# Kernel tuning notes

Hardware: AMD Instinct MI355X
Metric: run time of the kernel (lower is better)

Reference implementation:

```python
import jax, jax.numpy as jnp
import numpy as np

N = 64      # SSM state size (hidden_size)
H = 1024    # channels
L = 2048    # sequence length
BATCH = 8


def setup_inputs() -> dict:
    key = jax.random.key(0)
    ks = jax.random.split(key, 12)
    s = 1.0 / np.sqrt(N)
    n = jnp.arange(N, dtype=jnp.float32)
    return {
        "r": jax.random.normal(ks[0], (BATCH, L, H), dtype=jnp.float32),
        "B_re": jax.random.normal(ks[1], (N,), dtype=jnp.float32) * s,
        "B_im": jax.random.normal(ks[2], (N,), dtype=jnp.float32) * s,
        "C_re": jax.random.normal(ks[3], (H, N), dtype=jnp.float32) * s,
        "C_im": jax.random.normal(ks[4], (H, N), dtype=jnp.float32) * s,
        "P_re": jax.random.normal(ks[5], (N,), dtype=jnp.float32) * s,
        "P_im": jax.random.normal(ks[6], (N,), dtype=jnp.float32) * s,
        "Q_re": jax.random.normal(ks[7], (N,), dtype=jnp.float32) * s,
        "Q_im": jax.random.normal(ks[8], (N,), dtype=jnp.float32) * s,
        # HiPPO-LegS-like diagonal: negative real part for stability, imag ~ pi*n
        "diag_re": -0.5 * jnp.ones((N,), dtype=jnp.float32),
        "diag_im": jnp.pi * (n - N / 2.0),
        "step": jnp.array([1e-3], dtype=jnp.float32),
        "D": jnp.zeros((1,), dtype=jnp.float32),
    }


def _dplr_kernel(Bc, Cc, Pc, Qc, Lam, step, seq_len):
    # Standard S4 DPLR generating function evaluated at roots of unity,
    # then inverse FFT -> real convolution kernel K_c of shape (H, L).
    z = jnp.exp(-2j * jnp.pi * jnp.arange(seq_len) / seq_len).astype(jnp.complex64)  # (L,)
    g = (2.0 / step) * (1.0 - z) / (1.0 + z)                                          # (L,)
    cden = 1.0 / (g[:, None] - Lam[None, :])                                          # (L,N) Cauchy denom
    k00 = jnp.einsum('hn,ln->hl', Cc * Bc, cden)   # (H,L)
    k01 = jnp.einsum('hn,ln->hl', Cc * Pc, cden)   # (H,L)
    k10 = jnp.einsum('n,ln->l', Qc * Bc, cden)     # (L,)
    k11 = jnp.einsum('n,ln->l', Qc * Pc, cden)     # (L,)
    at_roots = (2.0 / (1.0 + z)) * (k00 - k01 * (k10 / (1.0 + k11)))  # (H,L)
    return jnp.fft.ifft(at_roots, axis=-1).real


def reference(r, B_re, B_im, C_re, C_im, P_re, P_im, Q_re, Q_im,
              diag_re, diag_im, step, D):
    step_c = jnp.maximum(step[0], 1e-6)
    Bc = B_re + 1j * B_im
    Cc = C_re + 1j * C_im
    Pc = P_re + 1j * P_im
    Qc = Q_re + 1j * Q_im
    Lam = diag_re + 1j * diag_im
    seq_len = r.shape[1]
    K = _dplr_kernel(Bc, Cc, Pc, Qc, Lam, step_c, seq_len)  # (H, L)
    # causal FFT convolution along the sequence axis
    nfft = 2 * seq_len
    Kf = jnp.fft.rfft(K, n=nfft, axis=-1)            # (H, nfft//2+1)
    uf = jnp.fft.rfft(r, n=nfft, axis=1)             # (B, nfft//2+1, H)
    h1 = jnp.fft.irfft(uf * Kf.T[None], n=nfft, axis=1)[:, :seq_len]  # (B,L,H)
    y1 = h1 + D[0] * r
    return jax.nn.gelu(y1, approximate=False)
```

## Files before the change

kernel.cpp:

```cpp
#include <hip/hip_runtime.h>
#include <math.h>

#define SSM_N 64
#define SSM_H 1024
#define SSM_L 2048
#define SSM_B 8
#define FFTN 2048
#define NT 256
#define NT2 512

#define PSWZ(a) ((a) ^ (((a) >> 4) & 15))

typedef float f2 __attribute__((ext_vector_type(2)));
static __device__ __forceinline__ f2 mkf2(float a, float b){ f2 v; v.x = a; v.y = b; return v; }

static __device__ __forceinline__ f2 cmul(f2 a, f2 b){
  return mkf2(-a.y, a.y) * mkf2(b.y, b.x) + mkf2(a.x, a.x) * b;
}
static __device__ __forceinline__ f2 cconj(f2 a){ return mkf2(a.x, -a.y); }

template<bool INV> static __device__ __forceinline__ f2 mul_mi(f2 a){
  return INV ? mkf2(-a.y, a.x) : mkf2(a.y, -a.x);
}
template<bool INV> static __device__ __forceinline__ f2 mul_w81(f2 a){
  const float r = 0.70710678118654752440f;
  return INV ? (r * mkf2(a.x - a.y, a.y + a.x)) : (r * mkf2(a.x + a.y, a.y - a.x));
}
template<bool INV> static __device__ __forceinline__ f2 mul_w83(f2 a){
  const float r = 0.70710678118654752440f;
  return INV ? (r * mkf2(-(a.x + a.y), a.x - a.y)) : (r * mkf2(a.y - a.x, -(a.x + a.y)));
}

#define W8C0 1.f
#define W8S0 0.f
#define W8C1 0.92387953251f
#define W8S1 (-0.38268343236f)
#define W8C2 0.70710678119f
#define W8S2 (-0.70710678119f)
#define W8C3 0.38268343236f
#define W8S3 (-0.92387953251f)
#define W8C4 0.f
#define W8S4 (-1.f)
#define W8C5 (-0.38268343236f)
#define W8S5 (-0.92387953251f)
#define W8C6 (-0.70710678119f)
#define W8S6 (-0.70710678119f)
#define W8C7 (-0.92387953251f)
#define W8S7 (-0.38268343236f)

template<bool INV>
static __device__ __forceinline__ void bfly8(const f2* x, f2* y)
{
  f2 t0=x[0]+x[4], t4=x[0]-x[4];
  f2 t1=x[1]+x[5], t5=x[1]-x[5];
  f2 t2=x[2]+x[6], t6=x[2]-x[6];
  f2 t3=x[3]+x[7], t7=x[3]-x[7];
  f2 b0=t0+t2, b2=t0-t2, b1=t1+t3, b3=t1-t3;
  f2 mb3 = mul_mi<INV>(b3);
  y[0]=b0+b1; y[4]=b0-b1; y[2]=b2+mb3; y[6]=b2-mb3;
  f2 v1 = mul_w81<INV>(t5), v2 = mul_mi<INV>(t6), v3 = mul_w83<INV>(t7);
  f2 a0=t4+v2, a2=t4-v2, a1=v1+v3, a3=v1-v3;
  f2 ma3 = mul_mi<INV>(a3);
  y[1]=a0+a1; y[5]=a0-a1; y[3]=a2+ma3; y[7]=a2-ma3;
}

template<bool INV>
static __device__ __forceinline__ void calc_w8(const f2* __restrict__ tw, int j, f2* w)
{
  f2 w1 = tw[j];
  if (INV) w1.y = -w1.y;
  w[1]=w1; w[2]=cmul(w1,w1); w[3]=cmul(w[2],w1); w[4]=cmul(w[2],w[2]);
  w[5]=cmul(w[3],w[2]); w[6]=cmul(w[3],w[3]); w[7]=cmul(w[4],w[3]);
}

static __device__ __forceinline__ void twstore(f2* __restrict__ dst, const f2* y, const f2* w,
                                               int base, int S)
{
  dst[PSWZ(base)]     = y[0];
  dst[PSWZ(base+S)]   = cmul(y[1],w[1]);
  dst[PSWZ(base+2*S)] = cmul(y[2],w[2]);
  dst[PSWZ(base+3*S)] = cmul(y[3],w[3]);
  dst[PSWZ(base+4*S)] = cmul(y[4],w[4]);
  dst[PSWZ(base+5*S)] = cmul(y[5],w[5]);
  dst[PSWZ(base+6*S)] = cmul(y[6],w[6]);
  dst[PSWZ(base+7*S)] = cmul(y[7],w[7]);
}

template<bool INV>
static __device__ __forceinline__ void bfly8_store(f2* __restrict__ dst, const f2* __restrict__ tw,
                                                   f2* x, int j, int base, int S)
{
  f2 y[8]; bfly8<INV>(x, y);
  f2 w[8]; calc_w8<INV>(tw, j, w);
  twstore(dst, y, w, base, S);
}

template<bool INV, bool ZTOP>
static __device__ __forceinline__ void stage8_first(const f2* __restrict__ src, f2* __restrict__ dst,
                                                    const f2* __restrict__ tw, int t, int st)
{
  const f2* sp = src + st;
  f2 x[8];
  if (ZTOP) {
    #pragma unroll
    for (int q = 0; q < 4; ++q) { x[q] = sp[256*q]; x[q+4] = mkf2(0.f, 0.f); }
  } else {
    #pragma unroll
    for (int q = 0; q < 8; ++q) x[q] = sp[256*q];
  }
  bfly8_store<INV>(dst, tw, x, t, t*8, 1);
}

template<bool INV, int S>
static __device__ __forceinline__ void stage8_mid(const f2* __restrict__ src, f2* __restrict__ dst,
                                                  const f2* __restrict__ tw, int t, int st)
{
  const f2* sp = src + st;
  f2 x[8];
  #pragma unroll
  for (int q = 0; q < 8; ++q) x[q] = sp[256*q];
  int i = t & (S-1);
  int j = t - i;
  bfly8_store<INV>(dst, tw, x, j, i + j*8, S);
}

template<bool INV, int S>
static __device__ __forceinline__ void stage8_mid_ip(f2* __restrict__ buf, const f2* __restrict__ tw,
                                                     int t, int st)
{
  f2 x[8];
  #pragma unroll
  for (int q = 0; q < 8; ++q) x[q] = buf[st + 256*q];
  __syncthreads();
  int i = t & (S-1);
  int j = t - i;
  bfly8_store<INV>(buf, tw, x, j, i + j*8, S);
  __syncthreads();
}

template<bool INV, bool HALFOUT>
static __device__ __forceinline__ void stage4f(const f2* __restrict__ src, f2* __restrict__ dst, int st)
{
  #pragma unroll
  for (int hh = 0; hh < 2; ++hh) {
    const f2* sp = src + st + 256*hh;
    f2* wp = dst + st + 256*hh;
    f2 x0=sp[0], x1=sp[512], x2=sp[1024], x3=sp[1536];
    f2 a0=x0+x2, a2=x0-x2, a1=x1+x3, a3=x1-x3;
    f2 m = mul_mi<INV>(a3);
    wp[0]   = a0+a1;
    wp[512] = a2+m;
    if (!HALFOUT) {
      wp[1024] = a0-a1;
      wp[1536] = a2-m;
    }
  }
}

template<bool INV>
static __device__ __forceinline__ void stage4f_ip(f2* __restrict__ buf, int st)
{
  f2 xr[2][4];
  #pragma unroll
  for (int hh = 0; hh < 2; ++hh) {
    const f2* sp = buf + st + 256*hh;
    xr[hh][0]=sp[0]; xr[hh][1]=sp[512]; xr[hh][2]=sp[1024]; xr[hh][3]=sp[1536];
  }
  __syncthreads();
  #pragma unroll
  for (int hh = 0; hh < 2; ++hh) {
    f2* wp = buf + st + 256*hh;
    f2 a0=xr[hh][0]+xr[hh][2], a2=xr[hh][0]-xr[hh][2];
    f2 a1=xr[hh][1]+xr[hh][3], a3=xr[hh][1]-xr[hh][3];
    f2 m = mul_mi<INV>(a3);
    wp[0]    = a0+a1;
    wp[512]  = a2+m;
    wp[1024] = a0-a1;
    wp[1536] = a2-m;
  }
  __syncthreads();
}

template<bool INV>
static __device__ __forceinline__ void stage4f_reg(const f2* __restrict__ src, f2* out, int st)
{
  #pragma unroll
  for (int hh = 0; hh < 2; ++hh) {
    const f2* sp = src + st + 256*hh;
    f2 x0=sp[0], x1=sp[512], x2=sp[1024], x3=sp[1536];
    f2 a0=x0+x2, a2=x0-x2, a1=x1+x3, a3=x1-x3;
    f2 m = mul_mi<INV>(a3);
    out[hh]   = a0+a1;
    out[hh+2] = a2+m;
    out[hh+4] = a0-a1;
    out[hh+6] = a2-m;
  }
}

static __device__ __forceinline__ f2 init_tw(f2* tw, int t)
{
  float s, c;
  sincosf(-6.2831853071795864769f * (float)t / (float)FFTN, &s, &c);
  f2 v = mkf2(c, s);
  tw[t] = v;
  return v;
}

__global__ __launch_bounds__(256) void kprep(
    const float* __restrict__ r, float* __restrict__ rT,
    const float* __restrict__ B_re, const float* __restrict__ B_im,
    const float* __restrict__ P_re, const float* __restrict__ P_im,
    const float* __restrict__ Q_re, const float* __restrict__ Q_im,
    const float* __restrict__ diag_re, const float* __restrict__ diag_im,
    const float* __restrict__ step,
    f2* __restrict__ cdenT, f2* __restrict__ f2v, f2* __restrict__ facv)
{
  __shared__ float til[64][65];
  int bid = blockIdx.x;
  int t = threadIdx.x;
  if (bid < 4096) {
    int tx = t & 15, ty = t >> 4;
    int h0 = (bid & 15) * 64, l0 = ((bid >> 4) & 31) * 64, b = bid >> 9;
    const float4* s4 = (const float4*)(r + ((size_t)b*SSM_L + l0)*SSM_H + h0);
    #pragma unroll
    for (int i = 0; i < 4; ++i) {
      int lr = ty + 16*i;
      float4 v = s4[(size_t)lr*(SSM_H/4) + tx];
      til[lr][4*tx+0]=v.x; til[lr][4*tx+1]=v.y; til[lr][4*tx+2]=v.z; til[lr][4*tx+3]=v.w;
    }
    __syncthreads();
    float4* d4 = (float4*)(rT + ((size_t)b*SSM_H + h0)*SSM_L + l0);
    #pragma unroll
    for (int i = 0; i < 4; ++i) {
      int hr = ty + 16*i;
      float4 w;
      w.x = til[4*tx+0][hr]; w.y = til[4*tx+1][hr];
      w.z = til[4*tx+2][hr]; w.w = til[4*tx+3][hr];
      d4[(size_t)hr*(SSM_L/4) + tx] = w;
    }
  } else {
    int gid = (bid - 4096) * 256 + t;
    int l = gid >> 3, s = gid & 7;
    double stepc = (double)step[0]; if (stepc < 1e-6) stepc = 1e-6;
    double ang = -2.0 * 3.14159265358979323846 * (double)l / (double)SSM_L;
    double zr = cos(ang), zi = sin(ang);
    double dr = 1.0 + zr, di = zi;
    double nr = 1.0 - zr, ni = -zi;
    double den = dr*dr + di*di;
    double i2s = 2.0 / stepc;
    double gr = i2s * (nr*dr + ni*di) / den;
    double gi = i2s * (ni*dr - nr*di) / den;
    double k10r=0.0, k10i=0.0, k11r=0.0, k11i=0.0;
    #pragma unroll
    for (int q = 0; q < 8; ++q) {
      int n = s*8 + q;
      double ar = gr - (double)diag_re[n];
      double ai = gi - (double)diag_im[n];
      double d2 = ar*ar + ai*ai;
      double cr = ar/d2, ci = -ai/d2;
      cdenT[n*SSM_L + l] = mkf2((float)cr, (float)ci);
      double qr = (double)Q_re[n], qi = (double)Q_im[n];
      double br = (double)B_re[n], bi = (double)B_im[n];
      double pr = (double)P_re[n], pi = (double)P_im[n];
      double qbr = qr*br - qi*bi, qbi = qr*bi + qi*br;
      double qpr = qr*pr - qi*pi, qpi = qr*pi + qi*pr;
      k10r += qbr*cr - qbi*ci; k10i += qbr*ci + qbi*cr;
      k11r += qpr*cr - qpi*ci; k11i += qpr*ci + qpi*cr;
    }
    #pragma unroll
    for (int off = 1; off < 8; off <<= 1) {
      k10r += __shfl_xor(k10r, off);
      k10i += __shfl_xor(k10i, off);
      k11r += __shfl_xor(k11r, off);
      k11i += __shfl_xor(k11i, off);
    }
    if (s == 0) {
      f2v[l] = mkf2((float)(2.0*dr/den), (float)(-2.0*di/den));
      double er = 1.0 + k11r, ei = k11i;
      double ed = er*er + ei*ei;
      facv[l] = mkf2((float)((k10r*er + k10i*ei)/ed), (float)((k10i*er - k10r*ei)/ed));
    }
  }
}

__global__ __launch_bounds__(NT2, 4) void kkern(
    const float* __restrict__ C_re, const float* __restrict__ C_im,
    const float* __restrict__ B_re, const float* __restrict__ B_im,
    const float* __restrict__ P_re, const float* __restrict__ P_im,
    const f2* __restrict__ cdenT, const f2* __restrict__ f2v, const f2* __restrict__ facv,
    float4* __restrict__ PQg)
{
  __shared__ f2 bufA[2][FFTN];
  __shared__ f2 bufB[2][FFTN];
  __shared__ f2 tw[256];
  int t = threadIdx.x;
  int tt = t & 255, ch = t >> 8, stt = PSWZ(tt);
  int h0 = blockIdx.x * 2;
  if (t < 256) init_tw(tw, t);
  f2* cbs = bufA[0];
  if (t < 128) {
    int h = h0 + (t >> 6), n = t & 63;
    f2 cc = mkf2(C_re[h*SSM_N + n], C_im[h*SSM_N + n]);
    cbs[t]       = cmul(cc, mkf2(B_re[n], B_im[n]));
    cbs[128 + t] = cmul(cc, mkf2(P_re[n], P_im[n]));
  }
  __syncthreads();
  f2 k00[2][4], k01[2][4];
  #pragma unroll
  for (int h2 = 0; h2 < 2; ++h2)
    #pragma unroll
    for (int i = 0; i < 4; ++i) { k00[h2][i] = mkf2(0.f,0.f); k01[h2][i] = mkf2(0.f,0.f); }
  f2 cd[4];
  #pragma unroll
  for (int i = 0; i < 4; ++i) cd[i] = cdenT[t + i*NT2];
  for (int n = 0; n < SSM_N; ++n) {
    f2 cdn[4];
    #pragma unroll
    for (int i = 0; i < 4; ++i) cdn[i] = cdenT[((n+1)&63)*SSM_L + t + i*NT2];
    #pragma unroll
    for (int h2 = 0; h2 < 2; ++h2) {
      f2 cb = cbs[h2*64 + n], cp = cbs[128 + h2*64 + n];
      #pragma unroll
      for (int i = 0; i < 4; ++i) {
        k00[h2][i] = k00[h2][i] + cmul(cb, cd[i]);
        k01[h2][i] = k01[h2][i] + cmul(cp, cd[i]);
      }
    }
    #pragma unroll
    for (int i = 0; i < 4; ++i) cd[i] = cdn[i];
  }
  __syncthreads();
  #pragma unroll
  for (int h2 = 0; h2 < 2; ++h2)
    #pragma unroll
    for (int i = 0; i < 4; ++i) {
      int l = t + i*NT2;
      f2 fv = f2v[l], fc = facv[l];
      bufA[h2][PSWZ(l)] = cmul(fv, k00[h2][i] - cmul(k01[h2][i], fc));
    }
  __syncthreads();
  f2* A  = bufA[ch];
  f2* Bb = bufB[ch];
  f2 ebin[4], e2048 = mkf2(0.f, 0.f);
  #pragma unroll
  for (int i = 0; i < 4; ++i) {
    int m = tt + i*256;
    if (m == 0) {
      ebin[0] = mkf2(A[0].x, 0.f);
      e2048   = mkf2(A[PSWZ(FFTN/2)].x, 0.f);
    } else {
      ebin[i] = 0.5f * (A[PSWZ(m)] + cconj(A[PSWZ(FFTN - m)]));
    }
  }
  stage8_first<true, false>(A, Bb, tw, tt, stt);
  __syncthreads();
  stage8_mid<true, 8>(Bb, A, tw, tt, stt);
  __syncthreads();
  stage8_mid<true, 64>(A, Bb, tw, tt, stt);
  __syncthreads();
  {
    f2 kr[8];
    stage4f_reg<true>(Bb, kr, stt);
    float sbb, cbb;
    sincosf(-3.14159265358979f * (float)tt / (float)FFTN, &sbb, &cbb);
    f2 cbase = mkf2(cbb, sbb);
    const float Wc8[8] = {W8C0,W8C1,W8C2,W8C3,W8C4,W8C5,W8C6,W8C7};
    const float Ws8[8] = {W8S0,W8S1,W8S2,W8S3,W8S4,W8S5,W8S6,W8S7};
    const float scale = 1.0f / (float)FFTN;
    #pragma unroll
    for (int q = 0; q < 8; ++q) {
      f2 tq = cmul(cbase, mkf2(Wc8[q], Ws8[q]));
      kr[q] = (kr[q].x * scale) * tq;
    }
    f2 w[8]; calc_w8<false>(tw, tt, w);
    f2 y[8]; bfly8<false>(kr, y); twstore(A, y, w, tt*8, 1);
  }
  __syncthreads();
  stage8_mid<false, 8>(A, Bb, tw, tt, stt);
  __syncthreads();
  stage8_mid<false, 64>(Bb, A, tw, tt, stt);
  __syncthreads();
  stage4f<false, true>(A, Bb, stt);
  #pragma unroll
  for (int i = 0; i < 4; ++i) {
    int m = tt + 256*i;
    f2 v = ebin[i];
    if (m == 0) v = e2048;
    Bb[1024 + m] = v;
  }
  __syncthreads();
  f2 u = tw[tt];
  const float q4 = 1.0f / 4096.0f;
  const f2 c1 = mkf2(0.99999882345170176f, -0.00153398018628477f);
  f2 base_odd = cmul(c1, u);
  const float Wc8[8] = {W8C0,W8C1,W8C2,W8C3,W8C4,W8C5,W8C6,W8C7};
  const float Ws8[8] = {W8S0,W8S1,W8S2,W8S3,W8S4,W8S5,W8S6,W8S7};
  float4* pqrow = PQg + (size_t)(h0 + ch) * FFTN;
  #pragma unroll
  for (int i = 0; i < 4; ++i) {
    int m = tt + 256*i;
    f2 Ka = ebin[i];
    f2 Kb = Bb[1024 + ((1024 - m) & 1023)];
    f2 ee = cmul(u, mkf2(Wc8[2*i], Ws8[2*i]));
    float cv = ee.x, sv = -ee.y;
    float am = q4*(1.f - sv), ap = q4*(1.f + sv), cq = q4*cv;
    f2 P = mkf2(Ka.x*am + Kb.x*ap, Ka.y*am - Kb.y*ap);
    f2 dd = mkf2(Ka.x - Kb.x, Ka.y + Kb.y);
    pqrow[2*m] = make_float4(P.x, P.y, -dd.y*cq, dd.x*cq);
    f2 Ko = Bb[PSWZ(m)];
    f2 Kp = Bb[PSWZ(1023 - m)];
    f2 eo = cmul(base_odd, mkf2(Wc8[2*i], Ws8[2*i]));
    cv = eo.x; sv = -eo.y;
    am = q4*(1.f - sv); ap = q4*(1.f + sv); cq = q4*cv;
    f2 P2 = mkf2(Ko.x*am + Kp.x*ap, Ko.y*am - Kp.y*ap);
    f2 d2 = mkf2(Ko.x - Kp.x, Ko.y + Kp.y);
    pqrow[2*m+1] = make_float4(P2.x, P2.y, -d2.y*cq, d2.x*cq);
  }
}

__global__ __launch_bounds__(NT, 4) void kconv(float* __restrict__ rT,
                                               const float4* __restrict__ PQg,
                                               const float* __restrict__ Dp)
{
  __shared__ f2 buf[FFTN];
  __shared__ f2 tw[256];
  int t = threadIdx.x, st = PSWZ(t);
  int xc = blockIdx.x & 7, y = blockIdx.x >> 3;
  int h = xc * 128 + (y >> 3);
  int b = y & 7;
  float Dv = Dp[0];
  init_tw(tw, t);
  float* rrow = rT + ((size_t)b*SSM_H + h) * SSM_L;
  const f2* r2 = (const f2*)rrow;
  f2 rv[4];
  #pragma unroll
  for (int i = 0; i < 4; ++i) rv[i] = r2[t + i*NT];
  {
    f2 xx[8];
    #pragma unroll
    for (int q = 0; q < 4; ++q) { xx[q] = rv[q]; xx[q+4] = mkf2(0.f, 0.f); }
    bfly8_store<false>(buf, tw, xx, t, t*8, 1);
  }
  __syncthreads();
  stage8_mid_ip<false, 8>(buf, tw, t, st);
  stage8_mid_ip<false, 64>(buf, tw, t, st);
  const float4* pqrow = PQg + (size_t)h * FFTN;
  float4 pq[8];
  #pragma unroll
  for (int i = 0; i < 8; ++i) pq[i] = pqrow[t + i*NT];
  stage4f_ip<false>(buf, st);
  {
    f2 xx[8];
    #pragma unroll
    for (int i = 0; i < 8; ++i) {
      int k = t + i*NT;
      int kk = (FFTN - k) & (FFTN - 1);
      f2 Ck  = buf[st + i*NT];
      f2 Ckk = buf[PSWZ(kk)];
      xx[i] = cmul(mkf2(pq[i].x, pq[i].y), Ck) + cmul(mkf2(pq[i].z, pq[i].w), cconj(Ckk));
    }
    __syncthreads();
    bfly8_store<true>(buf, tw, xx, t, t*8, 1);
  }
  __syncthreads();
  stage8_mid_ip<true, 8>(buf, tw, t, st);
  stage8_mid_ip<true, 64>(buf, tw, t, st);
  f2* o2 = (f2*)rrow;
  #pragma unroll
  for (int hh = 0; hh < 2; ++hh) {
    const f2* sp = buf + st + 256*hh;
    f2 x0=sp[0], x1=sp[512], x2=sp[1024], x3=sp[1536];
    f2 a0=x0+x2, a2=x0-x2, a1=x1+x3, a3=x1-x3;
    f2 mm = mul_mi<true>(a3);
    f2 y0 = a0+a1, y1 = a2+mm;
    f2 rA = rv[hh], rB = rv[hh+2];
    o2[t + 256*hh]       = mkf2(y0.x + Dv*rA.x, y0.y + Dv*rA.y);
    o2[t + 256*hh + 512] = mkf2(y1.x + Dv*rB.x, y1.y + Dv*rB.y);
  }
}

__global__ __launch_bounds__(256) void ktback(const float* __restrict__ yT, float* __restrict__ out)
{
  __shared__ float til[64][65];
  int t = threadIdx.x, tx = t & 15, ty = t >> 4;
  int h0 = blockIdx.x * 64, l0 = blockIdx.y * 64, b = blockIdx.z;
  const float4* s4 = (const float4*)(yT + ((size_t)b*SSM_H + h0)*SSM_L + l0);
  #pragma unroll
  for (int i = 0; i < 4; ++i) {
    int hr = ty + 16*i;
    float4 v = s4[(size_t)hr*(SSM_L/4) + tx];
    til[hr][4*tx+0]=v.x; til[hr][4*tx+1]=v.y; til[hr][4*tx+2]=v.z; til[hr][4*tx+3]=v.w;
  }
  __syncthreads();
  float4* d4 = (float4*)(out + ((size_t)b*SSM_L + l0)*SSM_H + h0);
  #pragma unroll
  for (int i = 0; i < 4; ++i) {
    int lr = ty + 16*i;
    float4 w;
    float x0 = til[4*tx+0][lr], x1 = til[4*tx+1][lr];
    float x2 = til[4*tx+2][lr], x3 = til[4*tx+3][lr];
    w.x = 0.5f * x0 * (1.0f + erff(x0 * 0.70710678118654752f));
    w.y = 0.5f * x1 * (1.0f + erff(x1 * 0.70710678118654752f));
    w.z = 0.5f * x2 * (1.0f + erff(x2 * 0.70710678118654752f));
    w.w = 0.5f * x3 * (1.0f + erff(x3 * 0.70710678118654752f));
    d4[(size_t)lr*(SSM_H/4) + tx] = w;
  }
}

extern "C" void kernel_launch(void* const* d_in, const int* in_sizes, int n_in,
                              void* d_out, int out_size, void* d_ws, size_t ws_size,
                              hipStream_t stream)
{
  const float* r       = (const float*)d_in[0];
  const float* B_re    = (const float*)d_in[1];
  const float* B_im    = (const float*)d_in[2];
  const float* C_re    = (const float*)d_in[3];
  const float* C_im    = (const float*)d_in[4];
  const float* P_re    = (const float*)d_in[5];
  const float* P_im    = (const float*)d_in[6];
  const float* Q_re    = (const float*)d_in[7];
  const float* Q_im    = (const float*)d_in[8];
  const float* diag_re = (const float*)d_in[9];
  const float* diag_im = (const float*)d_in[10];
  const float* step    = (const float*)d_in[11];
  const float* Dp      = (const float*)d_in[12];
  float* out = (float*)d_out;

  char* p = (char*)d_ws;
  float* rT  = (float*)p;  p += (size_t)SSM_B*SSM_H*SSM_L*sizeof(float);
  f2* cdenT  = (f2*)p;     p += (size_t)SSM_N*SSM_L*sizeof(f2);
  f2* f2v    = (f2*)p;     p += (size_t)SSM_L*sizeof(f2);
  f2* facv   = (f2*)p;     p += (size_t)SSM_L*sizeof(f2);
  float4* PQ = (float4*)p; p += (size_t)SSM_H*FFTN*sizeof(float4);

  kprep<<<4096 + 64, 256, 0, stream>>>(r, rT, B_re, B_im, P_re, P_im, Q_re, Q_im,
                                       diag_re, diag_im, step, cdenT, f2v, facv);
  kkern<<<SSM_H/2, NT2, 0, stream>>>(C_re, C_im, B_re, B_im, P_re, P_im,
                                     cdenT, f2v, facv, PQ);
  kconv<<<SSM_B*SSM_H, NT, 0, stream>>>(rT, PQ, Dp);
  ktback<<<dim3(SSM_H/64, SSM_L/64, SSM_B), 256, 0, stream>>>(rT, out);
}
```

Measured before the change: 264.7 us.

## Drop transpose kernels; read and write strided rows directly in conv kernel

```diff
diff --git a/kernel.cpp b/kernel.cpp
--- a/kernel.cpp
+++ b/kernel.cpp
@@ -207,7 +207,6 @@
 }
 
 __global__ __launch_bounds__(256) void kprep(
-    const float* __restrict__ r, float* __restrict__ rT,
     const float* __restrict__ B_re, const float* __restrict__ B_im,
     const float* __restrict__ P_re, const float* __restrict__ P_im,
     const float* __restrict__ Q_re, const float* __restrict__ Q_im,
@@ -215,71 +214,46 @@
     const float* __restrict__ step,
     f2* __restrict__ cdenT, f2* __restrict__ f2v, f2* __restrict__ facv)
 {
-  __shared__ float til[64][65];
-  int bid = blockIdx.x;
-  int t = threadIdx.x;
-  if (bid < 4096) {
-    int tx = t & 15, ty = t >> 4;
-    int h0 = (bid & 15) * 64, l0 = ((bid >> 4) & 31) * 64, b = bid >> 9;
-    const float4* s4 = (const float4*)(r + ((size_t)b*SSM_L + l0)*SSM_H + h0);
-    #pragma unroll
-    for (int i = 0; i < 4; ++i) {
-      int lr = ty + 16*i;
-      float4 v = s4[(size_t)lr*(SSM_H/4) + tx];
-      til[lr][4*tx+0]=v.x; til[lr][4*tx+1]=v.y; til[lr][4*tx+2]=v.z; til[lr][4*tx+3]=v.w;
-    }
-    __syncthreads();
-    float4* d4 = (float4*)(rT + ((size_t)b*SSM_H + h0)*SSM_L + l0);
-    #pragma unroll
-    for (int i = 0; i < 4; ++i) {
-      int hr = ty + 16*i;
-      float4 w;
-      w.x = til[4*tx+0][hr]; w.y = til[4*tx+1][hr];
-      w.z = til[4*tx+2][hr]; w.w = til[4*tx+3][hr];
-      d4[(size_t)hr*(SSM_L/4) + tx] = w;
-    }
-  } else {
-    int gid = (bid - 4096) * 256 + t;
-    int l = gid >> 3, s = gid & 7;
-    double stepc = (double)step[0]; if (stepc < 1e-6) stepc = 1e-6;
-    double ang = -2.0 * 3.14159265358979323846 * (double)l / (double)SSM_L;
-    double zr = cos(ang), zi = sin(ang);
-    double dr = 1.0 + zr, di = zi;
-    double nr = 1.0 - zr, ni = -zi;
-    double den = dr*dr + di*di;
-    double i2s = 2.0 / stepc;
-    double gr = i2s * (nr*dr + ni*di) / den;
-    double gi = i2s * (ni*dr - nr*di) / den;
-    double k10r=0.0, k10i=0.0, k11r=0.0, k11i=0.0;
-    #pragma unroll
-    for (int q = 0; q < 8; ++q) {
-      int n = s*8 + q;
-      double ar = gr - (double)diag_re[n];
-      double ai = gi - (double)diag_im[n];
-      double d2 = ar*ar + ai*ai;
-      double cr = ar/d2, ci = -ai/d2;
-      cdenT[n*SSM_L + l] = mkf2((float)cr, (float)ci);
-      double qr = (double)Q_re[n], qi = (double)Q_im[n];
-      double br = (double)B_re[n], bi = (double)B_im[n];
-      double pr = (double)P_re[n], pi = (double)P_im[n];
-      double qbr = qr*br - qi*bi, qbi = qr*bi + qi*br;
-      double qpr = qr*pr - qi*pi, qpi = qr*pi + qi*pr;
-      k10r += qbr*cr - qbi*ci; k10i += qbr*ci + qbi*cr;
-      k11r += qpr*cr - qpi*ci; k11i += qpr*ci + qpi*cr;
-    }
-    #pragma unroll
-    for (int off = 1; off < 8; off <<= 1) {
-      k10r += __shfl_xor(k10r, off);
-      k10i += __shfl_xor(k10i, off);
-      k11r += __shfl_xor(k11r, off);
-      k11i += __shfl_xor(k11i, off);
-    }
-    if (s == 0) {
-      f2v[l] = mkf2((float)(2.0*dr/den), (float)(-2.0*di/den));
-      double er = 1.0 + k11r, ei = k11i;
-      double ed = er*er + ei*ei;
-      facv[l] = mkf2((float)((k10r*er + k10i*ei)/ed), (float)((k10i*er - k10r*ei)/ed));
-    }
+  int gid = blockIdx.x * 256 + threadIdx.x;
+  int l = gid >> 3, s = gid & 7;
+  double stepc = (double)step[0]; if (stepc < 1e-6) stepc = 1e-6;
+  double ang = -2.0 * 3.14159265358979323846 * (double)l / (double)SSM_L;
+  double zr = cos(ang), zi = sin(ang);
+  double dr = 1.0 + zr, di = zi;
+  double nr = 1.0 - zr, ni = -zi;
+  double den = dr*dr + di*di;
+  double i2s = 2.0 / stepc;
+  double gr = i2s * (nr*dr + ni*di) / den;
+  double gi = i2s * (ni*dr - nr*di) / den;
+  double k10r=0.0, k10i=0.0, k11r=0.0, k11i=0.0;
+  #pragma unroll
+  for (int q = 0; q < 8; ++q) {
+    int n = s*8 + q;
+    double ar = gr - (double)diag_re[n];
+    double ai = gi - (double)diag_im[n];
+    double d2 = ar*ar + ai*ai;
+    double cr = ar/d2, ci = -ai/d2;
+    cdenT[n*SSM_L + l] = mkf2((float)cr, (float)ci);
+    double qr = (double)Q_re[n], qi = (double)Q_im[n];
+    double br = (double)B_re[n], bi = (double)B_im[n];
+    double pr = (double)P_re[n], pi = (double)P_im[n];
+    double qbr = qr*br - qi*bi, qbi = qr*bi + qi*br;
+    double qpr = qr*pr - qi*pi, qpi = qr*pi + qi*pr;
+    k10r += qbr*cr - qbi*ci; k10i += qbr*ci + qbi*cr;
+    k11r += qpr*cr - qpi*ci; k11i += qpr*ci + qpi*cr;
+  }
+  #pragma unroll
+  for (int off = 1; off < 8; off <<= 1) {
+    k10r += __shfl_xor(k10r, off);
+    k10i += __shfl_xor(k10i, off);
+    k11r += __shfl_xor(k11r, off);
+    k11i += __shfl_xor(k11i, off);
+  }
+  if (s == 0) {
+    f2v[l] = mkf2((float)(2.0*dr/den), (float)(-2.0*di/den));
+    double er = 1.0 + k11r, ei = k11i;
+    double ed = er*er + ei*ei;
+    facv[l] = mkf2((float)((k10r*er + k10i*ei)/ed), (float)((k10i*er - k10r*ei)/ed));
   }
 }
 
@@ -418,23 +392,26 @@
   }
 }
 
-__global__ __launch_bounds__(NT, 4) void kconv(float* __restrict__ rT,
+__global__ __launch_bounds__(NT, 4) void kconv(const float* __restrict__ r,
                                                const float4* __restrict__ PQg,
-                                               const float* __restrict__ Dp)
+                                               const float* __restrict__ Dp,
+                                               float* __restrict__ out)
 {
   __shared__ f2 buf[FFTN];
   __shared__ f2 tw[256];
   int t = threadIdx.x, st = PSWZ(t);
-  int xc = blockIdx.x & 7, y = blockIdx.x >> 3;
-  int h = xc * 128 + (y >> 3);
-  int b = y & 7;
+  int xcd = blockIdx.x & 7, local = blockIdx.x >> 3;
+  int h = (xcd << 7) | (local & 127);
+  int b = local >> 7;
   float Dv = Dp[0];
+  const float* rp = r + (size_t)b * SSM_L * SSM_H + h;
+  f2 rv[4];
+  #pragma unroll
+  for (int i = 0; i < 4; ++i) {
+    int j2 = t + i*NT;
+    rv[i] = mkf2(rp[(size_t)(2*j2) * SSM_H], rp[(size_t)(2*j2 + 1) * SSM_H]);
+  }
   init_tw(tw, t);
-  float* rrow = rT + ((size_t)b*SSM_H + h) * SSM_L;
-  const f2* r2 = (const f2*)rrow;
-  f2 rv[4];
-  #pragma unroll
-  for (int i = 0; i < 4; ++i) rv[i] = r2[t + i*NT];
   {
     f2 xx[8];
     #pragma unroll
@@ -465,7 +442,8 @@
   __syncthreads();
   stage8_mid_ip<true, 8>(buf, tw, t, st);
   stage8_mid_ip<true, 64>(buf, tw, t, st);
-  f2* o2 = (f2*)rrow;
+  float* op = out + (size_t)b * SSM_L * SSM_H + h;
+  const float kq = 0.70710678118654752f;
   #pragma unroll
   for (int hh = 0; hh < 2; ++hh) {
     const f2* sp = buf + st + 256*hh;
@@ -474,36 +452,13 @@
     f2 mm = mul_mi<true>(a3);
     f2 y0 = a0+a1, y1 = a2+mm;
     f2 rA = rv[hh], rB = rv[hh+2];
-    o2[t + 256*hh]       = mkf2(y0.x + Dv*rA.x, y0.y + Dv*rA.y);
-    o2[t + 256*hh + 512] = mkf2(y1.x + Dv*rB.x, y1.y + Dv*rB.y);
-  }
-}
-
-__global__ __launch_bounds__(256) void ktback(const float* __restrict__ yT, float* __restrict__ out)
-{
-  __shared__ float til[64][65];
-  int t = threadIdx.x, tx = t & 15, ty = t >> 4;
-  int h0 = blockIdx.x * 64, l0 = blockIdx.y * 64, b = blockIdx.z;
-  const float4* s4 = (const float4*)(yT + ((size_t)b*SSM_H + h0)*SSM_L + l0);
-  #pragma unroll
-  for (int i = 0; i < 4; ++i) {
-    int hr = ty + 16*i;
-    float4 v = s4[(size_t)hr*(SSM_L/4) + tx];
-    til[hr][4*tx+0]=v.x; til[hr][4*tx+1]=v.y; til[hr][4*tx+2]=v.z; til[hr][4*tx+3]=v.w;
-  }
-  __syncthreads();
-  float4* d4 = (float4*)(out + ((size_t)b*SSM_L + l0)*SSM_H + h0);
-  #pragma unroll
-  for (int i = 0; i < 4; ++i) {
-    int lr = ty + 16*i;
-    float4 w;
-    float x0 = til[4*tx+0][lr], x1 = til[4*tx+1][lr];
-    float x2 = til[4*tx+2][lr], x3 = til[4*tx+3][lr];
-    w.x = 0.5f * x0 * (1.0f + erff(x0 * 0.70710678118654752f));
-    w.y = 0.5f * x1 * (1.0f + erff(x1 * 0.70710678118654752f));
-    w.z = 0.5f * x2 * (1.0f + erff(x2 * 0.70710678118654752f));
-    w.w = 0.5f * x3 * (1.0f + erff(x3 * 0.70710678118654752f));
-    d4[(size_t)lr*(SSM_H/4) + tx] = w;
+    int j0 = t + 256*hh, j1 = t + 256*hh + 512;
+    float v0 = y0.x + Dv*rA.x, v1 = y0.y + Dv*rA.y;
+    float v2 = y1.x + Dv*rB.x, v3 = y1.y + Dv*rB.y;
+    op[(size_t)(2*j0    ) * SSM_H] = 0.5f * v0 * (1.0f + erff(v0 * kq));
+    op[(size_t)(2*j0 + 1) * SSM_H] = 0.5f * v1 * (1.0f + erff(v1 * kq));
+    op[(size_t)(2*j1    ) * SSM_H] = 0.5f * v2 * (1.0f + erff(v2 * kq));
+    op[(size_t)(2*j1 + 1) * SSM_H] = 0.5f * v3 * (1.0f + erff(v3 * kq));
   }
 }
 
@@ -527,16 +482,14 @@
   float* out = (float*)d_out;
 
   char* p = (char*)d_ws;
-  float* rT  = (float*)p;  p += (size_t)SSM_B*SSM_H*SSM_L*sizeof(float);
   f2* cdenT  = (f2*)p;     p += (size_t)SSM_N*SSM_L*sizeof(f2);
   f2* f2v    = (f2*)p;     p += (size_t)SSM_L*sizeof(f2);
   f2* facv   = (f2*)p;     p += (size_t)SSM_L*sizeof(f2);
   float4* PQ = (float4*)p; p += (size_t)SSM_H*FFTN*sizeof(float4);
 
-  kprep<<<4096 + 64, 256, 0, stream>>>(r, rT, B_re, B_im, P_re, P_im, Q_re, Q_im,
-                                       diag_re, diag_im, step, cdenT, f2v, facv);
+  kprep<<<64, 256, 0, stream>>>(B_re, B_im, P_re, P_im, Q_re, Q_im,
+                                diag_re, diag_im, step, cdenT, f2v, facv);
   kkern<<<SSM_H/2, NT2, 0, stream>>>(C_re, C_im, B_re, B_im, P_re, P_im,
                                      cdenT, f2v, facv, PQ);
-  kconv<<<SSM_B*SSM_H, NT, 0, stream>>>(rT, PQ, Dp);
-  ktback<<<dim3(SSM_H/64, SSM_L/64, SSM_B), 256, 0, stream>>>(rT, out);
-}
+  kconv<<<SSM_B*SSM_H, NT, 0, stream>>>(r, PQ, Dp, out);
+}
```

After: 305.1 us. +15.3%, slower.

## Move input transpose into kernel-generation launch to overlap memory and compute work

Applied to the files above, without the earlier changes.

```diff
diff --git a/kernel.cpp b/kernel.cpp
--- a/kernel.cpp
+++ b/kernel.cpp
@@ -207,7 +207,6 @@
 }
 
 __global__ __launch_bounds__(256) void kprep(
-    const float* __restrict__ r, float* __restrict__ rT,
     const float* __restrict__ B_re, const float* __restrict__ B_im,
     const float* __restrict__ P_re, const float* __restrict__ P_im,
     const float* __restrict__ Q_re, const float* __restrict__ Q_im,
@@ -215,87 +214,93 @@
     const float* __restrict__ step,
     f2* __restrict__ cdenT, f2* __restrict__ f2v, f2* __restrict__ facv)
 {
-  __shared__ float til[64][65];
-  int bid = blockIdx.x;
-  int t = threadIdx.x;
-  if (bid < 4096) {
-    int tx = t & 15, ty = t >> 4;
-    int h0 = (bid & 15) * 64, l0 = ((bid >> 4) & 31) * 64, b = bid >> 9;
-    const float4* s4 = (const float4*)(r + ((size_t)b*SSM_L + l0)*SSM_H + h0);
-    #pragma unroll
-    for (int i = 0; i < 4; ++i) {
-      int lr = ty + 16*i;
-      float4 v = s4[(size_t)lr*(SSM_H/4) + tx];
-      til[lr][4*tx+0]=v.x; til[lr][4*tx+1]=v.y; til[lr][4*tx+2]=v.z; til[lr][4*tx+3]=v.w;
-    }
-    __syncthreads();
-    float4* d4 = (float4*)(rT + ((size_t)b*SSM_H + h0)*SSM_L + l0);
-    #pragma unroll
-    for (int i = 0; i < 4; ++i) {
-      int hr = ty + 16*i;
-      float4 w;
-      w.x = til[4*tx+0][hr]; w.y = til[4*tx+1][hr];
-      w.z = til[4*tx+2][hr]; w.w = til[4*tx+3][hr];
-      d4[(size_t)hr*(SSM_L/4) + tx] = w;
-    }
-  } else {
-    int gid = (bid - 4096) * 256 + t;
-    int l = gid >> 3, s = gid & 7;
-    double stepc = (double)step[0]; if (stepc < 1e-6) stepc = 1e-6;
-    double ang = -2.0 * 3.14159265358979323846 * (double)l / (double)SSM_L;
-    double zr = cos(ang), zi = sin(ang);
-    double dr = 1.0 + zr, di = zi;
-    double nr = 1.0 - zr, ni = -zi;
-    double den = dr*dr + di*di;
-    double i2s = 2.0 / stepc;
-    double gr = i2s * (nr*dr + ni*di) / den;
-    double gi = i2s * (ni*dr - nr*di) / den;
-    double k10r=0.0, k10i=0.0, k11r=0.0, k11i=0.0;
-    #pragma unroll
-    for (int q = 0; q < 8; ++q) {
-      int n = s*8 + q;
-      double ar = gr - (double)diag_re[n];
-      double ai = gi - (double)diag_im[n];
-      double d2 = ar*ar + ai*ai;
-      double cr = ar/d2, ci = -ai/d2;
-      cdenT[n*SSM_L + l] = mkf2((float)cr, (float)ci);
-      double qr = (double)Q_re[n], qi = (double)Q_im[n];
-      double br = (double)B_re[n], bi = (double)B_im[n];
-      double pr = (double)P_re[n], pi = (double)P_im[n];
-      double qbr = qr*br - qi*bi, qbi = qr*bi + qi*br;
-      double qpr = qr*pr - qi*pi, qpi = qr*pi + qi*pr;
-      k10r += qbr*cr - qbi*ci; k10i += qbr*ci + qbi*cr;
-      k11r += qpr*cr - qpi*ci; k11i += qpr*ci + qpi*cr;
-    }
-    #pragma unroll
-    for (int off = 1; off < 8; off <<= 1) {
-      k10r += __shfl_xor(k10r, off);
-      k10i += __shfl_xor(k10i, off);
-      k11r += __shfl_xor(k11r, off);
-      k11i += __shfl_xor(k11i, off);
-    }
-    if (s == 0) {
-      f2v[l] = mkf2((float)(2.0*dr/den), (float)(-2.0*di/den));
-      double er = 1.0 + k11r, ei = k11i;
-      double ed = er*er + ei*ei;
-      facv[l] = mkf2((float)((k10r*er + k10i*ei)/ed), (float)((k10i*er - k10r*ei)/ed));
-    }
-  }
-}
-
-__global__ __launch_bounds__(NT2, 4) void kkern(
+  int gid = blockIdx.x * 256 + threadIdx.x;
+  int l = gid >> 3, s = gid & 7;
+  double stepc = (double)step[0]; if (stepc < 1e-6) stepc = 1e-6;
+  double ang = -2.0 * 3.14159265358979323846 * (double)l / (double)SSM_L;
+  double zr = cos(ang), zi = sin(ang);
+  double dr = 1.0 + zr, di = zi;
+  double nr = 1.0 - zr, ni = -zi;
+  double den = dr*dr + di*di;
+  double i2s = 2.0 / stepc;
+  double gr = i2s * (nr*dr + ni*di) / den;
+  double gi = i2s * (ni*dr - nr*di) / den;
+  double k10r=0.0, k10i=0.0, k11r=0.0, k11i=0.0;
+  #pragma unroll
+  for (int q = 0; q < 8; ++q) {
+    int n = s*8 + q;
+    double ar = gr - (double)diag_re[n];
+    double ai = gi - (double)diag_im[n];
+    double d2 = ar*ar + ai*ai;
+    double cr = ar/d2, ci = -ai/d2;
+    cdenT[n*SSM_L + l] = mkf2((float)cr, (float)ci);
+    double qr = (double)Q_re[n], qi = (double)Q_im[n];
+    double br = (double)B_re[n], bi = (double)B_im[n];
+    double pr = (double)P_re[n], pi = (double)P_im[n];
+    double qbr = qr*br - qi*bi, qbi = qr*bi + qi*br;
+    double qpr = qr*pr - qi*pi, qpi = qr*pi + qi*pr;
+    k10r += qbr*cr - qbi*ci; k10i += qbr*ci + qbi*cr;
+    k11r += qpr*cr - qpi*ci; k11i += qpr*ci + qpi*cr;
+  }
+  #pragma unroll
+  for (int off = 1; off < 8; off <<= 1) {
+    k10r += __shfl_xor(k10r, off);
+    k10i += __shfl_xor(k10i, off);
+    k11r += __shfl_xor(k11r, off);
+    k11i += __shfl_xor(k11i, off);
+  }
+  if (s == 0) {
+    f2v[l] = mkf2((float)(2.0*dr/den), (float)(-2.0*di/den));
+    double er = 1.0 + k11r, ei = k11i;
+    double ed = er*er + ei*ei;
+    facv[l] = mkf2((float)((k10r*er + k10i*ei)/ed), (float)((k10i*er - k10r*ei)/ed));
+  }
+}
+
+__global__ __launch_bounds__(NT2, 4) void kmid(
+    const float* __restrict__ r, float* __restrict__ rT,
     const float* __restrict__ C_re, const float* __restrict__ C_im,
     const float* __restrict__ B_re, const float* __restrict__ B_im,
     const float* __restrict__ P_re, const float* __restrict__ P_im,
     const f2* __restrict__ cdenT, const f2* __restrict__ f2v, const f2* __restrict__ facv,
     float4* __restrict__ PQg)
 {
-  __shared__ f2 bufA[2][FFTN];
-  __shared__ f2 bufB[2][FFTN];
-  __shared__ f2 tw[256];
+  __shared__ f2 smem[4*FFTN + 256];
+  int bid = blockIdx.x;
   int t = threadIdx.x;
+  int nk = bid / 5, rem = bid - nk*5;
+  if (rem != 0) {
+    float (*til)[64][65] = (float (*)[64][65])smem;
+    int sub = t >> 8, tt = t & 255;
+    int td = (nk*4 + rem - 1)*2 + sub;
+    int tx = tt & 15, ty = tt >> 4;
+    int h0 = (td & 15) * 64, l0 = ((td >> 4) & 31) * 64, b = td >> 9;
+    const float4* s4 = (const float4*)(r + ((size_t)b*SSM_L + l0)*SSM_H + h0);
+    #pragma unroll
+    for (int i = 0; i < 4; ++i) {
+      int lr = ty + 16*i;
+      float4 v = s4[(size_t)lr*(SSM_H/4) + tx];
+      til[sub][lr][4*tx+0]=v.x; til[sub][lr][4*tx+1]=v.y;
+      til[sub][lr][4*tx+2]=v.z; til[sub][lr][4*tx+3]=v.w;
+    }
+    __syncthreads();
+    float4* d4 = (float4*)(rT + ((size_t)b*SSM_H + h0)*SSM_L + l0);
+    #pragma unroll
+    for (int i = 0; i < 4; ++i) {
+      int hr = ty + 16*i;
+      float4 w;
+      w.x = til[sub][4*tx+0][hr]; w.y = til[sub][4*tx+1][hr];
+      w.z = til[sub][4*tx+2][hr]; w.w = til[sub][4*tx+3][hr];
+      d4[(size_t)hr*(SSM_L/4) + tx] = w;
+    }
+    return;
+  }
+  f2* sb = smem;
+  f2 (*bufA)[FFTN] = reinterpret_cast<f2 (*)[FFTN]>(sb);
+  f2 (*bufB)[FFTN] = reinterpret_cast<f2 (*)[FFTN]>(sb + 2*FFTN);
+  f2* tw = sb + 4*FFTN;
   int tt = t & 255, ch = t >> 8, stt = PSWZ(tt);
-  int h0 = blockIdx.x * 2;
+  int h0 = nk * 2;
   if (t < 256) init_tw(tw, t);
   f2* cbs = bufA[0];
   if (t < 128) {
@@ -533,10 +538,10 @@
   f2* facv   = (f2*)p;     p += (size_t)SSM_L*sizeof(f2);
   float4* PQ = (float4*)p; p += (size_t)SSM_H*FFTN*sizeof(float4);
 
-  kprep<<<4096 + 64, 256, 0, stream>>>(r, rT, B_re, B_im, P_re, P_im, Q_re, Q_im,
-                                       diag_re, diag_im, step, cdenT, f2v, facv);
-  kkern<<<SSM_H/2, NT2, 0, stream>>>(C_re, C_im, B_re, B_im, P_re, P_im,
-                                     cdenT, f2v, facv, PQ);
+  kprep<<<64, 256, 0, stream>>>(B_re, B_im, P_re, P_im, Q_re, Q_im,
+                                diag_re, diag_im, step, cdenT, f2v, facv);
+  kmid<<<2560, NT2, 0, stream>>>(r, rT, C_re, C_im, B_re, B_im, P_re, P_im,
+                                 cdenT, f2v, facv, PQ);
   kconv<<<SSM_B*SSM_H, NT, 0, stream>>>(rT, PQ, Dp);
   ktback<<<dim3(SSM_H/64, SSM_L/64, SSM_B), 256, 0, stream>>>(rT, out);
 }
```

After: 276.5 us. +4.4%, slower.

## Overlap input transpose with kernel-generation FFT in one interleaved launch

Applied to the files above, without the earlier changes.

```diff
diff --git a/kernel.cpp b/kernel.cpp
--- a/kernel.cpp
+++ b/kernel.cpp
@@ -7,7 +7,6 @@
 #define SSM_B 8
 #define FFTN 2048
 #define NT 256
-#define NT2 512
 
 #define PSWZ(a) ((a) ^ (((a) >> 4) & 15))
 
@@ -95,35 +94,6 @@
   twstore(dst, y, w, base, S);
 }
 
-template<bool INV, bool ZTOP>
-static __device__ __forceinline__ void stage8_first(const f2* __restrict__ src, f2* __restrict__ dst,
-                                                    const f2* __restrict__ tw, int t, int st)
-{
-  const f2* sp = src + st;
-  f2 x[8];
-  if (ZTOP) {
-    #pragma unroll
-    for (int q = 0; q < 4; ++q) { x[q] = sp[256*q]; x[q+4] = mkf2(0.f, 0.f); }
-  } else {
-    #pragma unroll
-    for (int q = 0; q < 8; ++q) x[q] = sp[256*q];
-  }
-  bfly8_store<INV>(dst, tw, x, t, t*8, 1);
-}
-
-template<bool INV, int S>
-static __device__ __forceinline__ void stage8_mid(const f2* __restrict__ src, f2* __restrict__ dst,
-                                                  const f2* __restrict__ tw, int t, int st)
-{
-  const f2* sp = src + st;
-  f2 x[8];
-  #pragma unroll
-  for (int q = 0; q < 8; ++q) x[q] = sp[256*q];
-  int i = t & (S-1);
-  int j = t - i;
-  bfly8_store<INV>(dst, tw, x, j, i + j*8, S);
-}
-
 template<bool INV, int S>
 static __device__ __forceinline__ void stage8_mid_ip(f2* __restrict__ buf, const f2* __restrict__ tw,
                                                      int t, int st)
@@ -136,25 +106,6 @@
   int j = t - i;
   bfly8_store<INV>(buf, tw, x, j, i + j*8, S);
   __syncthreads();
-}
-
-template<bool INV, bool HALFOUT>
-static __device__ __forceinline__ void stage4f(const f2* __restrict__ src, f2* __restrict__ dst, int st)
-{
-  #pragma unroll
-  for (int hh = 0; hh < 2; ++hh) {
-    const f2* sp = src + st + 256*hh;
-    f2* wp = dst + st + 256*hh;
-    f2 x0=sp[0], x1=sp[512], x2=sp[1024], x3=sp[1536];
-    f2 a0=x0+x2, a2=x0-x2, a1=x1+x3, a3=x1-x3;
-    f2 m = mul_mi<INV>(a3);
-    wp[0]   = a0+a1;
-    wp[512] = a2+m;
-    if (!HALFOUT) {
-      wp[1024] = a0-a1;
-      wp[1536] = a2-m;
-    }
-  }
 }
 
 template<bool INV>
@@ -207,7 +158,6 @@
 }
 
 __global__ __launch_bounds__(256) void kprep(
-    const float* __restrict__ r, float* __restrict__ rT,
     const float* __restrict__ B_re, const float* __restrict__ B_im,
     const float* __restrict__ P_re, const float* __restrict__ P_im,
     const float* __restrict__ Q_re, const float* __restrict__ Q_im,
@@ -215,12 +165,66 @@
     const float* __restrict__ step,
     f2* __restrict__ cdenT, f2* __restrict__ f2v, f2* __restrict__ facv)
 {
-  __shared__ float til[64][65];
+  int gid = blockIdx.x * 256 + threadIdx.x;
+  int l = gid >> 3, s = gid & 7;
+  double stepc = (double)step[0]; if (stepc < 1e-6) stepc = 1e-6;
+  double ang = -2.0 * 3.14159265358979323846 * (double)l / (double)SSM_L;
+  double zr = cos(ang), zi = sin(ang);
+  double dr = 1.0 + zr, di = zi;
+  double nr = 1.0 - zr, ni = -zi;
+  double den = dr*dr + di*di;
+  double i2s = 2.0 / stepc;
+  double gr = i2s * (nr*dr + ni*di) / den;
+  double gi = i2s * (ni*dr - nr*di) / den;
+  double k10r=0.0, k10i=0.0, k11r=0.0, k11i=0.0;
+  #pragma unroll
+  for (int q = 0; q < 8; ++q) {
+    int n = s*8 + q;
+    double ar = gr - (double)diag_re[n];
+    double ai = gi - (double)diag_im[n];
+    double d2 = ar*ar + ai*ai;
+    double cr = ar/d2, ci = -ai/d2;
+    cdenT[n*SSM_L + l] = mkf2((float)cr, (float)ci);
+    double qr = (double)Q_re[n], qi = (double)Q_im[n];
+    double br = (double)B_re[n], bi = (double)B_im[n];
+    double pr = (double)P_re[n], pi = (double)P_im[n];
+    double qbr = qr*br - qi*bi, qbi = qr*bi + qi*br;
+    double qpr = qr*pr - qi*pi, qpi = qr*pi + qi*pr;
+    k10r += qbr*cr - qbi*ci; k10i += qbr*ci + qbi*cr;
+    k11r += qpr*cr - qpi*ci; k11i += qpr*ci + qpi*cr;
+  }
+  #pragma unroll
+  for (int off = 1; off < 8; off <<= 1) {
+    k10r += __shfl_xor(k10r, off);
+    k10i += __shfl_xor(k10i, off);
+    k11r += __shfl_xor(k11r, off);
+    k11i += __shfl_xor(k11i, off);
+  }
+  if (s == 0) {
+    f2v[l] = mkf2((float)(2.0*dr/den), (float)(-2.0*di/den));
+    double er = 1.0 + k11r, ei = k11i;
+    double ed = er*er + ei*ei;
+    facv[l] = mkf2((float)((k10r*er + k10i*ei)/ed), (float)((k10i*er - k10r*ei)/ed));
+  }
+}
+
+__global__ __launch_bounds__(NT, 3) void kmid(
+    const float* __restrict__ r, float* __restrict__ rT,
+    const float* __restrict__ C_re, const float* __restrict__ C_im,
+    const float* __restrict__ B_re, const float* __restrict__ B_im,
+    const float* __restrict__ P_re, const float* __restrict__ P_im,
+    const f2* __restrict__ cdenT, const f2* __restrict__ f2v, const f2* __restrict__ facv,
+    float4* __restrict__ PQg)
+{
+  __shared__ f2 smem[FFTN + 256];
   int bid = blockIdx.x;
   int t = threadIdx.x;
-  if (bid < 4096) {
+  int nk = bid / 5, rem = bid - nk*5;
+  if (rem != 0) {
+    float (*til)[65] = (float (*)[65])smem;
+    int td = nk*4 + rem - 1;
     int tx = t & 15, ty = t >> 4;
-    int h0 = (bid & 15) * 64, l0 = ((bid >> 4) & 31) * 64, b = bid >> 9;
+    int h0 = (td & 15) * 64, l0 = ((td >> 4) & 31) * 64, b = td >> 9;
     const float4* s4 = (const float4*)(r + ((size_t)b*SSM_L + l0)*SSM_H + h0);
     #pragma unroll
     for (int i = 0; i < 4; ++i) {
@@ -238,131 +242,63 @@
       w.z = til[4*tx+2][hr]; w.w = til[4*tx+3][hr];
       d4[(size_t)hr*(SSM_L/4) + tx] = w;
     }
-  } else {
-    int gid = (bid - 4096) * 256 + t;
-    int l = gid >> 3, s = gid & 7;
-    double stepc = (double)step[0]; if (stepc < 1e-6) stepc = 1e-6;
-    double ang = -2.0 * 3.14159265358979323846 * (double)l / (double)SSM_L;
-    double zr = cos(ang), zi = sin(ang);
-    double dr = 1.0 + zr, di = zi;
-    double nr = 1.0 - zr, ni = -zi;
-    double den = dr*dr + di*di;
-    double i2s = 2.0 / stepc;
-    double gr = i2s * (nr*dr + ni*di) / den;
-    double gi = i2s * (ni*dr - nr*di) / den;
-    double k10r=0.0, k10i=0.0, k11r=0.0, k11i=0.0;
-    #pragma unroll
-    for (int q = 0; q < 8; ++q) {
-      int n = s*8 + q;
-      double ar = gr - (double)diag_re[n];
-      double ai = gi - (double)diag_im[n];
-      double d2 = ar*ar + ai*ai;
-      double cr = ar/d2, ci = -ai/d2;
-      cdenT[n*SSM_L + l] = mkf2((float)cr, (float)ci);
-      double qr = (double)Q_re[n], qi = (double)Q_im[n];
-      double br = (double)B_re[n], bi = (double)B_im[n];
-      double pr = (double)P_re[n], pi = (double)P_im[n];
-      double qbr = qr*br - qi*bi, qbi = qr*bi + qi*br;
-      double qpr = qr*pr - qi*pi, qpi = qr*pi + qi*pr;
-      k10r += qbr*cr - qbi*ci; k10i += qbr*ci + qbi*cr;
-      k11r += qpr*cr - qpi*ci; k11i += qpr*ci + qpi*cr;
-    }
-    #pragma unroll
-    for (int off = 1; off < 8; off <<= 1) {
-      k10r += __shfl_xor(k10r, off);
-      k10i += __shfl_xor(k10i, off);
-      k11r += __shfl_xor(k11r, off);
-      k11i += __shfl_xor(k11i, off);
-    }
-    if (s == 0) {
-      f2v[l] = mkf2((float)(2.0*dr/den), (float)(-2.0*di/den));
-      double er = 1.0 + k11r, ei = k11i;
-      double ed = er*er + ei*ei;
-      facv[l] = mkf2((float)((k10r*er + k10i*ei)/ed), (float)((k10i*er - k10r*ei)/ed));
-    }
-  }
-}
-
-__global__ __launch_bounds__(NT2, 4) void kkern(
-    const float* __restrict__ C_re, const float* __restrict__ C_im,
-    const float* __restrict__ B_re, const float* __restrict__ B_im,
-    const float* __restrict__ P_re, const float* __restrict__ P_im,
-    const f2* __restrict__ cdenT, const f2* __restrict__ f2v, const f2* __restrict__ facv,
-    float4* __restrict__ PQg)
-{
-  __shared__ f2 bufA[2][FFTN];
-  __shared__ f2 bufB[2][FFTN];
-  __shared__ f2 tw[256];
-  int t = threadIdx.x;
-  int tt = t & 255, ch = t >> 8, stt = PSWZ(tt);
-  int h0 = blockIdx.x * 2;
-  if (t < 256) init_tw(tw, t);
-  f2* cbs = bufA[0];
+    return;
+  }
+  f2* buf = smem;
+  f2* tw  = smem + FFTN;
+  int st = PSWZ(t);
+  int h = nk;
+  init_tw(tw, t);
+  f2* cbs = buf;
   if (t < 128) {
-    int h = h0 + (t >> 6), n = t & 63;
+    int n = t & 63;
     f2 cc = mkf2(C_re[h*SSM_N + n], C_im[h*SSM_N + n]);
-    cbs[t]       = cmul(cc, mkf2(B_re[n], B_im[n]));
-    cbs[128 + t] = cmul(cc, mkf2(P_re[n], P_im[n]));
-  }
-  __syncthreads();
-  f2 k00[2][4], k01[2][4];
-  #pragma unroll
-  for (int h2 = 0; h2 < 2; ++h2)
-    #pragma unroll
-    for (int i = 0; i < 4; ++i) { k00[h2][i] = mkf2(0.f,0.f); k01[h2][i] = mkf2(0.f,0.f); }
-  f2 cd[4];
-  #pragma unroll
-  for (int i = 0; i < 4; ++i) cd[i] = cdenT[t + i*NT2];
+    cbs[t] = (t < 64) ? cmul(cc, mkf2(B_re[n], B_im[n]))
+                      : cmul(cc, mkf2(P_re[n], P_im[n]));
+  }
+  __syncthreads();
+  f2 k00[8], k01[8];
+  #pragma unroll
+  for (int i = 0; i < 8; ++i) { k00[i] = mkf2(0.f,0.f); k01[i] = mkf2(0.f,0.f); }
   for (int n = 0; n < SSM_N; ++n) {
-    f2 cdn[4];
-    #pragma unroll
-    for (int i = 0; i < 4; ++i) cdn[i] = cdenT[((n+1)&63)*SSM_L + t + i*NT2];
-    #pragma unroll
-    for (int h2 = 0; h2 < 2; ++h2) {
-      f2 cb = cbs[h2*64 + n], cp = cbs[128 + h2*64 + n];
-      #pragma unroll
-      for (int i = 0; i < 4; ++i) {
-        k00[h2][i] = k00[h2][i] + cmul(cb, cd[i]);
-        k01[h2][i] = k01[h2][i] + cmul(cp, cd[i]);
-      }
-    }
-    #pragma unroll
-    for (int i = 0; i < 4; ++i) cd[i] = cdn[i];
-  }
-  __syncthreads();
-  #pragma unroll
-  for (int h2 = 0; h2 < 2; ++h2)
-    #pragma unroll
-    for (int i = 0; i < 4; ++i) {
-      int l = t + i*NT2;
-      f2 fv = f2v[l], fc = facv[l];
-      bufA[h2][PSWZ(l)] = cmul(fv, k00[h2][i] - cmul(k01[h2][i], fc));
-    }
-  __syncthreads();
-  f2* A  = bufA[ch];
-  f2* Bb = bufB[ch];
+    f2 cb = cbs[n], cp = cbs[64 + n];
+    #pragma unroll
+    for (int i = 0; i < 8; ++i) {
+      f2 cd = cdenT[n*SSM_L + t + i*NT];
+      k00[i] = k00[i] + cmul(cb, cd);
+      k01[i] = k01[i] + cmul(cp, cd);
+    }
+  }
+  __syncthreads();
+  f2 ar[8];
+  #pragma unroll
+  for (int i = 0; i < 8; ++i) {
+    int l = t + i*NT;
+    ar[i] = cmul(f2v[l], k00[i] - cmul(k01[i], facv[l]));
+    buf[PSWZ(l)] = ar[i];
+  }
+  __syncthreads();
   f2 ebin[4], e2048 = mkf2(0.f, 0.f);
   #pragma unroll
   for (int i = 0; i < 4; ++i) {
-    int m = tt + i*256;
+    int m = t + i*NT;
     if (m == 0) {
-      ebin[0] = mkf2(A[0].x, 0.f);
-      e2048   = mkf2(A[PSWZ(FFTN/2)].x, 0.f);
+      ebin[0] = mkf2(buf[0].x, 0.f);
+      e2048   = mkf2(buf[PSWZ(FFTN/2)].x, 0.f);
     } else {
-      ebin[i] = 0.5f * (A[PSWZ(m)] + cconj(A[PSWZ(FFTN - m)]));
-    }
-  }
-  stage8_first<true, false>(A, Bb, tw, tt, stt);
-  __syncthreads();
-  stage8_mid<true, 8>(Bb, A, tw, tt, stt);
-  __syncthreads();
-  stage8_mid<true, 64>(A, Bb, tw, tt, stt);
-  __syncthreads();
+      ebin[i] = 0.5f * (buf[PSWZ(m)] + cconj(buf[PSWZ(FFTN - m)]));
+    }
+  }
+  __syncthreads();
+  bfly8_store<true>(buf, tw, ar, t, t*8, 1);
+  __syncthreads();
+  stage8_mid_ip<true, 8>(buf, tw, t, st);
+  stage8_mid_ip<true, 64>(buf, tw, t, st);
+  f2 kr[8];
+  stage4f_reg<true>(buf, kr, st);
   {
-    f2 kr[8];
-    stage4f_reg<true>(Bb, kr, stt);
     float sbb, cbb;
-    sincosf(-3.14159265358979f * (float)tt / (float)FFTN, &sbb, &cbb);
+    sincosf(-3.14159265358979f * (float)t / (float)FFTN, &sbb, &cbb);
     f2 cbase = mkf2(cbb, sbb);
     const float Wc8[8] = {W8C0,W8C1,W8C2,W8C3,W8C4,W8C5,W8C6,W8C7};
     const float Ws8[8] = {W8S0,W8S1,W8S2,W8S3,W8S4,W8S5,W8S6,W8S7};
@@ -372,43 +308,58 @@
       f2 tq = cmul(cbase, mkf2(Wc8[q], Ws8[q]));
       kr[q] = (kr[q].x * scale) * tq;
     }
-    f2 w[8]; calc_w8<false>(tw, tt, w);
-    f2 y[8]; bfly8<false>(kr, y); twstore(A, y, w, tt*8, 1);
-  }
-  __syncthreads();
-  stage8_mid<false, 8>(A, Bb, tw, tt, stt);
-  __syncthreads();
-  stage8_mid<false, 64>(Bb, A, tw, tt, stt);
-  __syncthreads();
-  stage4f<false, true>(A, Bb, stt);
-  #pragma unroll
-  for (int i = 0; i < 4; ++i) {
-    int m = tt + 256*i;
-    f2 v = ebin[i];
-    if (m == 0) v = e2048;
-    Bb[1024 + m] = v;
-  }
-  __syncthreads();
-  f2 u = tw[tt];
+  }
+  __syncthreads();
+  bfly8_store<false>(buf, tw, kr, t, t*8, 1);
+  __syncthreads();
+  stage8_mid_ip<false, 8>(buf, tw, t, st);
+  stage8_mid_ip<false, 64>(buf, tw, t, st);
+  {
+    f2 xr[2][4];
+    #pragma unroll
+    for (int hh = 0; hh < 2; ++hh) {
+      const f2* sp = buf + st + 256*hh;
+      xr[hh][0]=sp[0]; xr[hh][1]=sp[512]; xr[hh][2]=sp[1024]; xr[hh][3]=sp[1536];
+    }
+    __syncthreads();
+    #pragma unroll
+    for (int hh = 0; hh < 2; ++hh) {
+      f2* wp = buf + st + 256*hh;
+      f2 a0=xr[hh][0]+xr[hh][2], a2=xr[hh][0]-xr[hh][2];
+      f2 a1=xr[hh][1]+xr[hh][3], a3=xr[hh][1]-xr[hh][3];
+      f2 m = mul_mi<false>(a3);
+      wp[0]   = a0+a1;
+      wp[512] = a2+m;
+    }
+    #pragma unroll
+    for (int i = 0; i < 4; ++i) {
+      int m = t + 256*i;
+      f2 v = ebin[i];
+      if (m == 0) v = e2048;
+      buf[1024 + m] = v;
+    }
+  }
+  __syncthreads();
+  f2 u = tw[t];
   const float q4 = 1.0f / 4096.0f;
   const f2 c1 = mkf2(0.99999882345170176f, -0.00153398018628477f);
   f2 base_odd = cmul(c1, u);
   const float Wc8[8] = {W8C0,W8C1,W8C2,W8C3,W8C4,W8C5,W8C6,W8C7};
   const float Ws8[8] = {W8S0,W8S1,W8S2,W8S3,W8S4,W8S5,W8S6,W8S7};
-  float4* pqrow = PQg + (size_t)(h0 + ch) * FFTN;
+  float4* pqrow = PQg + (size_t)h * FFTN;
   #pragma unroll
   for (int i = 0; i < 4; ++i) {
-    int m = tt + 256*i;
+    int m = t + 256*i;
     f2 Ka = ebin[i];
-    f2 Kb = Bb[1024 + ((1024 - m) & 1023)];
+    f2 Kb = buf[1024 + ((1024 - m) & 1023)];
     f2 ee = cmul(u, mkf2(Wc8[2*i], Ws8[2*i]));
     float cv = ee.x, sv = -ee.y;
     float am = q4*(1.f - sv), ap = q4*(1.f + sv), cq = q4*cv;
     f2 P = mkf2(Ka.x*am + Kb.x*ap, Ka.y*am - Kb.y*ap);
     f2 dd = mkf2(Ka.x - Kb.x, Ka.y + Kb.y);
     pqrow[2*m] = make_float4(P.x, P.y, -dd.y*cq, dd.x*cq);
-    f2 Ko = Bb[PSWZ(m)];
-    f2 Kp = Bb[PSWZ(1023 - m)];
+    f2 Ko = buf[PSWZ(m)];
+    f2 Kp = buf[PSWZ(1023 - m)];
     f2 eo = cmul(base_odd, mkf2(Wc8[2*i], Ws8[2*i]));
     cv = eo.x; sv = -eo.y;
     am = q4*(1.f - sv); ap = q4*(1.f + sv); cq = q4*cv;
@@ -533,10 +484,10 @@
   f2* facv   = (f2*)p;     p += (size_t)SSM_L*sizeof(f2);
   float4* PQ = (float4*)p; p += (size_t)SSM_H*FFTN*sizeof(float4);
 
-  kprep<<<4096 + 64, 256, 0, stream>>>(r, rT, B_re, B_im, P_re, P_im, Q_re, Q_im,
-                                       diag_re, diag_im, step, cdenT, f2v, facv);
-  kkern<<<SSM_H/2, NT2, 0, stream>>>(C_re, C_im, B_re, B_im, P_re, P_im,
-                                     cdenT, f2v, facv, PQ);
+  kprep<<<64, 256, 0, stream>>>(B_re, B_im, P_re, P_im, Q_re, Q_im,
+                                diag_re, diag_im, step, cdenT, f2v, facv);
+  kmid<<<5120, NT, 0, stream>>>(r, rT, C_re, C_im, B_re, B_im, P_re, P_im,
+                                cdenT, f2v, facv, PQ);
   kconv<<<SSM_B*SSM_H, NT, 0, stream>>>(rT, PQ, Dp);
   ktback<<<dim3(SSM_H/64, SSM_L/64, SSM_B), 256, 0, stream>>>(rT, out);
 }
```

Result: slower. 308.4 us (+16.5%).
